# Performance work log

Measured on AMD Instinct MI355X. Metric: run time of the kernel, lower is better.

Reference implementation:

```python
import jax, jax.numpy as jnp
import numpy as np

N_NODES = 50000
N_EDGES = 800000
NODE_IN = 5
EDGE_IN = 1
HID = 64


def setup_inputs() -> dict:
    key = jax.random.key(0)
    ks = jax.random.split(key, 16)
    x = jax.random.normal(ks[0], (N_NODES, NODE_IN), dtype=jnp.float32)
    edge_index = jax.random.randint(ks[1], (2, N_EDGES), 0, N_NODES, dtype=jnp.int32)
    edge_attr = jax.random.normal(ks[2], (N_EDGES, EDGE_IN), dtype=jnp.float32)
    def lin(k, fan_in, fan_out):
        b = 1.0 / np.sqrt(fan_in)
        k1, k2 = jax.random.split(k)
        W = jax.random.uniform(k1, (fan_in, fan_out), minval=-b, maxval=b, dtype=jnp.float32)
        bi = jax.random.uniform(k2, (fan_out,), minval=-b, maxval=b, dtype=jnp.float32)
        return W, bi
    W_ne, b_ne = lin(ks[3], NODE_IN, HID)
    W_ee, b_ee = lin(ks[4], EDGE_IN, HID)
    W_gcn, b_gcn = lin(ks[5], HID, HID)   # PyG GCNConv: lin (no bias) + separate bias
    W1, b1 = lin(ks[6], 3 * HID, HID)
    W2, b2 = lin(ks[7], HID, 1)
    return {"x": x, "edge_index": edge_index, "edge_attr": edge_attr,
            "W_ne": W_ne, "b_ne": b_ne, "W_ee": W_ee, "b_ee": b_ee,
            "W_gcn": W_gcn, "b_gcn": b_gcn, "W1": W1, "b1": b1, "W2": W2, "b2": b2}


def gcn_conv(h, edge_index, W, b):
    # PyG GCNConv: add self-loops, symmetric norm D^-1/2 (A+I) D^-1/2, linear, scatter-add.
    N = h.shape[0]
    src, dst = edge_index[0], edge_index[1]
    loops = jnp.arange(N, dtype=src.dtype)
    row = jnp.concatenate([src, loops])  # message sources
    col = jnp.concatenate([dst, loops])  # message targets
    deg = jax.ops.segment_sum(jnp.ones(col.shape[0], h.dtype), col, num_segments=N)
    dinv = jnp.where(deg > 0, jax.lax.rsqrt(deg), 0.0)
    norm = dinv[row] * dinv[col]          # [E+N]
    ht = h @ W                            # [N, HID]
    msg = ht[row] * norm[:, None]         # gather + scale
    return jax.ops.segment_sum(msg, col, num_segments=N) + b


def reference(x, edge_index, edge_attr, W_ne, b_ne, W_ee, b_ee, W_gcn, b_gcn, W1, b1, W2, b2):
    h = jax.nn.relu(x @ W_ne + b_ne)                    # node encoder
    ef = jax.nn.relu(edge_attr @ W_ee + b_ee)           # edge encoder
    h = gcn_conv(h, edge_index, W_gcn, b_gcn)           # GCN layer
    src, dst = edge_index[0], edge_index[1]
    edge_input = jnp.concatenate([h[src], h[dst], ef], axis=1)  # [E, 3*HID]
    out = jax.nn.relu(edge_input @ W1 + b1) @ W2 + b2   # edge MLP -> [E, 1]
    return out.reshape(-1)
```

## Files before the change

kernel.cpp:

```cpp
#include <hip/hip_runtime.h>

#define NN 50000
#define NE 800000
#define H  64
#define NBKT 196
#define BCAP 8192
#define BIN_CHUNK 2048

typedef __attribute__((ext_vector_type(8))) short bf16x8;
typedef __attribute__((ext_vector_type(4))) float f32x4;

__device__ __forceinline__ unsigned short f2bf(float f) {
  unsigned int u = __builtin_bit_cast(unsigned int, f);
  u += 0x7FFFu + ((u >> 16) & 1u);
  return (unsigned short)(u >> 16);
}
__device__ __forceinline__ float bf2f(unsigned short u) {
  unsigned int v = ((unsigned int)u) << 16;
  return __builtin_bit_cast(float, v);
}

__global__ __launch_bounds__(256) void k_prep(
    const float* __restrict__ W1, const float* __restrict__ b1,
    const float* __restrict__ W_ee, const float* __restrict__ b_ee,
    float* __restrict__ thrS, float* __restrict__ cT,
    unsigned short* __restrict__ w1f, int* __restrict__ gcur) {
  const int t = threadIdx.x;
  if (blockIdx.x == 2) {
    if (t < NBKT) gcur[t] = 0;
    return;
  }
  if (blockIdx.x == 1) {
    const int ln = t & 63, q = t >> 6;
    const int l15_ = ln & 15, l4_ = ln >> 4;
#pragma unroll
    for (int f = 0; f < 4; ++f) {
      const int idx = q * 4 + f;
      const int g = idx >> 3;
      const int ct = (idx >> 1) & 3;
      const int c = idx & 1;
#pragma unroll
      for (int j = 0; j < 8; ++j) {
        const int k = g * 64 + c * 32 + l4_ * 8 + j;
        const int hcol = ct * 16 + l15_;
        w1f[(idx * 64 + ln) * 8 + j] = f2bf(W1[k * H + hcol]);
      }
    }
    return;
  }
  __shared__ float swee[64], sbee[64], sth[64];
  __shared__ int skx[64];
  if (t < 64) {
    const float w = W_ee[t], b = b_ee[t];
    swee[t] = w; sbee[t] = b;
    sth[t] = (w != 0.f) ? (-b / w) : __builtin_inff();
    skx[t] = t;
  }
  __syncthreads();
  for (int sz = 2; sz <= 64; sz <<= 1)
    for (int st = sz >> 1; st > 0; st >>= 1) {
      if (t < 64) {
        const int p = t ^ st;
        if (p > t) {
          const bool up = ((t & sz) == 0);
          const float a = sth[t], bb = sth[p];
          if (up ? (a > bb) : (a < bb)) {
            const int ka = skx[t];
            sth[t] = bb; sth[p] = a;
            skx[t] = skx[p]; skx[p] = ka;
          }
        }
      }
      __syncthreads();
    }
  if (t < 64) {
    const int h = t;
    float c1 = 0.f, c0 = b1[h];
    for (int k = 0; k < 64; ++k) {
      const float w = swee[k], b = sbee[k];
      if (w < 0.f || (w == 0.f && b > 0.f)) {
        const float wv1 = W1[(128 + k) * H + h];
        c1 = fmaf(w, wv1, c1);
        c0 = fmaf(b, wv1, c0);
      }
    }
    float2* cT2 = (float2*)cT;
    cT2[h] = make_float2(c1, c0);
    for (int iv = 1; iv <= 64; ++iv) {
      const int ks = skx[iv - 1];
      const float w = swee[ks];
      const float s = (w > 0.f) ? 1.f : -1.f;
      const float wv1 = W1[(128 + ks) * H + h];
      c1 = fmaf(s * w, wv1, c1);
      c0 = fmaf(s * sbee[ks], wv1, c0);
      cT2[iv * 66 + h] = make_float2(c1, c0);
    }
    thrS[h] = sth[h];
  }
}

__global__ __launch_bounds__(256) void k_bin(const int* __restrict__ ei,
                                             unsigned int* __restrict__ gbin,
                                             int* __restrict__ gcur) {
  __shared__ int hist[NBKT], base[NBKT];
  const int t = threadIdx.x;
  if (t < NBKT) hist[t] = 0;
  __syncthreads();

  const int e0 = blockIdx.x * BIN_CHUNK;
  int srcv[8], dstv[8], loff[8];
#pragma unroll
  for (int j = 0; j < 8; ++j) {
    const int e = e0 + j * 256 + t;
    if (e < NE) {
      srcv[j] = ei[e];
      dstv[j] = ei[NE + e];
      loff[j] = atomicAdd(&hist[dstv[j] >> 8], 1);
    } else dstv[j] = -1;
  }
  __syncthreads();
  if (t < NBKT) base[t] = atomicAdd(&gcur[t], hist[t]);
  __syncthreads();
#pragma unroll
  for (int j = 0; j < 8; ++j) {
    if (dstv[j] >= 0) {
      const int b = dstv[j] >> 8;
      const int pos = base[b] + loff[j];
      if (pos < BCAP)
        gbin[(size_t)b * BCAP + pos] =
            ((unsigned int)srcv[j] << 8) | (unsigned int)(dstv[j] & 255);
    }
  }
}

__global__ __launch_bounds__(256) void k_pass2(const unsigned int* __restrict__ gbin,
                                               const int* __restrict__ gcur,
                                               unsigned short* __restrict__ gcsr,
                                               int2* __restrict__ rowrange,
                                               float* __restrict__ dinv) {
  __shared__ int hist[256], cur[256], sc[256];
  __shared__ unsigned short lcsr[BCAP];
  const int b = blockIdx.x, t = threadIdx.x;
  const int sz = min(gcur[b], BCAP);
  hist[t] = 0;
  __syncthreads();

  const unsigned int* bb = gbin + (size_t)b * BCAP;
  for (int i = t; i < sz; i += 256) atomicAdd(&hist[bb[i] & 255], 1);
  __syncthreads();

  int v = hist[t];
  const int cnt = v;
  sc[t] = v;
  __syncthreads();
#pragma unroll
  for (int off = 1; off < 256; off <<= 1) {
    const int o = (t >= off) ? sc[t - off] : 0;
    __syncthreads();
    v += o;
    sc[t] = v;
    __syncthreads();
  }
  const int ex = v - cnt;
  cur[t] = ex;
  const int d = b * 256 + t;
  if (d < NN) {
    const int beg = b * BCAP + ex;
    rowrange[d] = make_int2(beg, beg + cnt);
    dinv[d] = rsqrtf((float)(cnt + 1));
  }
  __syncthreads();

  for (int i = t; i < sz; i += 256) {
    const unsigned int en = bb[i];
    const int off = atomicAdd(&cur[en & 255], 1);
    lcsr[off] = (unsigned short)(en >> 8);
  }
  __syncthreads();
  for (int i = t; i < sz; i += 256) gcsr[(size_t)b * BCAP + i] = lcsr[i];
}

__global__ __launch_bounds__(256) void k_node(
    const float* __restrict__ x, const float* __restrict__ W_ne,
    const float* __restrict__ b_ne, const float* __restrict__ W_gcn,
    const float* __restrict__ dinv, unsigned short* __restrict__ htb) {
  __shared__ float sh[4][H];
  const int lane = threadIdx.x & 63;
  const int wv   = threadIdx.x >> 6;
  const int n    = blockIdx.x * 4 + wv;

  float acc = b_ne[lane];
#pragma unroll
  for (int k = 0; k < 5; ++k) acc = fmaf(x[n * 5 + k], W_ne[k * H + lane], acc);
  acc = fmaxf(acc, 0.0f);
  sh[wv][lane] = acc;
  __syncthreads();

  float hv = 0.0f;
#pragma unroll 8
  for (int k = 0; k < H; ++k) hv = fmaf(sh[wv][k], W_gcn[k * H + lane], hv);

  htb[(size_t)n * H + lane] = f2bf(hv * dinv[n]);
}

__global__ __launch_bounds__(256) void k_gather(
    const int2* __restrict__ rowrange, const unsigned short* __restrict__ gcsr,
    const unsigned short* __restrict__ htb, const float* __restrict__ dinv,
    const float* __restrict__ b_gcn, unsigned short* __restrict__ hgb) {
  const int lane = threadIdx.x & 63;
  const int wv   = threadIdx.x >> 6;
  const int n    = blockIdx.x * 4 + wv;
  const int2 rr = rowrange[n];

  float sum = bf2f(htb[(size_t)n * H + lane]);
  int i = rr.x;
#pragma unroll 1
  for (; i + 4 <= rr.y; i += 4) {
    const int s0 = gcsr[i], s1 = gcsr[i + 1];
    const int s2 = gcsr[i + 2], s3 = gcsr[i + 3];
    const float v0 = bf2f(htb[(size_t)s0 * H + lane]);
    const float v1 = bf2f(htb[(size_t)s1 * H + lane]);
    const float v2 = bf2f(htb[(size_t)s2 * H + lane]);
    const float v3 = bf2f(htb[(size_t)s3 * H + lane]);
    sum += (v0 + v1) + (v2 + v3);
  }
#pragma unroll 1
  for (; i < rr.y; ++i) sum += bf2f(htb[(size_t)gcsr[i] * H + lane]);

  hgb[(size_t)n * H + lane] = f2bf(fmaf(dinv[n], sum, b_gcn[lane]));
}

__global__ __launch_bounds__(256) void k_uv(const unsigned short* __restrict__ hgb,
                                            const unsigned short* __restrict__ w1f,
                                            unsigned short* __restrict__ u,
                                            unsigned short* __restrict__ v) {
  const int lane = threadIdx.x & 63;
  const int wv   = threadIdx.x >> 6;
  const int tile = blockIdx.x * 4 + wv;
  if (tile >= NN / 16) return;
  const int n0 = tile * 16;
  const int l15 = lane & 15, l4 = lane >> 4;

  const unsigned short* ap = hgb + (size_t)(n0 + l15) * H + l4 * 8;
  const bf16x8 a0 = *(const bf16x8*)(ap);
  const bf16x8 a1 = *(const bf16x8*)(ap + 32);

  bf16x8 bU[4][2], bV[4][2];
#pragma unroll
  for (int ct = 0; ct < 4; ++ct)
#pragma unroll
    for (int c = 0; c < 2; ++c) {
      bU[ct][c] = *(const bf16x8*)(w1f + ((0 + ct * 2 + c) * 64 + lane) * 8);
      bV[ct][c] = *(const bf16x8*)(w1f + ((8 + ct * 2 + c) * 64 + lane) * 8);
    }

  f32x4 au[4], av[4];
#pragma unroll
  for (int ct = 0; ct < 4; ++ct) {
    au[ct] = (f32x4)(0.f);
    av[ct] = (f32x4)(0.f);
    au[ct] = __builtin_amdgcn_mfma_f32_16x16x32_bf16(a0, bU[ct][0], au[ct], 0, 0, 0);
    au[ct] = __builtin_amdgcn_mfma_f32_16x16x32_bf16(a1, bU[ct][1], au[ct], 0, 0, 0);
    av[ct] = __builtin_amdgcn_mfma_f32_16x16x32_bf16(a0, bV[ct][0], av[ct], 0, 0, 0);
    av[ct] = __builtin_amdgcn_mfma_f32_16x16x32_bf16(a1, bV[ct][1], av[ct], 0, 0, 0);
  }

#pragma unroll
  for (int ct = 0; ct < 4; ++ct)
#pragma unroll
    for (int r = 0; r < 4; ++r) {
      const size_t idx = (size_t)(n0 + l4 * 4 + r) * H + ct * 16 + l15;
      u[idx] = f2bf(au[ct][r]);
      v[idx] = f2bf(av[ct][r]);
    }
}

#define ET 5
__global__ __launch_bounds__(256) void k_edge(
    const int* __restrict__ ei, const float* __restrict__ eattr,
    const unsigned short* __restrict__ u, const unsigned short* __restrict__ v,
    const float* __restrict__ thrS, const float* __restrict__ cT,
    const float* __restrict__ W2, const float* __restrict__ b2,
    float* __restrict__ out) {
  __shared__ float sThr[64];
  __shared__ float sCT[65 * 132];

  const int t = threadIdx.x;
  if (t < 64) sThr[t] = thrS[t];
  for (int i = t; i < 65 * 66; i += 256)
    ((float2*)sCT)[i] = ((const float2*)cT)[i];
  __syncthreads();

  const int lane = t & 63;
  const int wv   = t >> 6;
  const int l15  = lane & 15, l4 = lane >> 4;
  const float b2v = b2[0];

  float w2v[16];
#pragma unroll
  for (int j = 0; j < 16; ++j) w2v[j] = W2[l4 * 16 + j];

  const int tile0 = (blockIdx.x * 4 + wv) * ET;
#pragma unroll 1
  for (int tt = 0; tt < ET; ++tt) {
    const int eBase = (tile0 + tt) * 16;
    const int src = ei[eBase + l15];
    const int dst = ei[NE + eBase + l15];
    const float ea = eattr[eBase + l15];

    unsigned int ud[8], vd[8];
    {
      const unsigned short* up = u + (size_t)src * H + l4 * 16;
      const unsigned short* vp = v + (size_t)dst * H + l4 * 16;
      *(uint4*)(ud)     = *(const uint4*)(up);
      *(uint4*)(ud + 4) = *(const uint4*)(up + 8);
      *(uint4*)(vd)     = *(const uint4*)(vp);
      *(uint4*)(vd + 4) = *(const uint4*)(vp + 8);
    }

    int iv = 0;
#pragma unroll
    for (int st = 64; st >= 1; st >>= 1) {
      const int nc = iv + st;
      if (nc <= 64 && sThr[nc - 1] <= ea) iv = nc;
    }

    const float* cp = sCT + iv * 132 + l4 * 32;
    float p = 0.0f;
#pragma unroll
    for (int r = 0; r < 8; ++r) {
      const float4 cc = *(const float4*)(cp + r * 4);
      const float ulo = __builtin_bit_cast(float, ud[r] << 16);
      const float uhi = __builtin_bit_cast(float, ud[r] & 0xFFFF0000u);
      const float vlo = __builtin_bit_cast(float, vd[r] << 16);
      const float vhi = __builtin_bit_cast(float, vd[r] & 0xFFFF0000u);
      const float z0 = ulo + vlo + fmaf(ea, cc.x, cc.y);
      const float z1 = uhi + vhi + fmaf(ea, cc.z, cc.w);
      p = fmaf(fmaxf(z0, 0.f), w2v[2 * r], p);
      p = fmaf(fmaxf(z1, 0.f), w2v[2 * r + 1], p);
    }

    p += __shfl_xor(p, 16);
    p += __shfl_xor(p, 32);
    if (lane < 16) out[eBase + lane] = p + b2v;
  }
}

extern "C" void kernel_launch(void* const* d_in, const int* in_sizes, int n_in,
                              void* d_out, int out_size, void* d_ws, size_t ws_size,
                              hipStream_t stream) {
  const float* x     = (const float*)d_in[0];
  const int*   ei    = (const int*)d_in[1];
  const float* eattr = (const float*)d_in[2];
  const float* W_ne  = (const float*)d_in[3];
  const float* b_ne  = (const float*)d_in[4];
  const float* W_ee  = (const float*)d_in[5];
  const float* b_ee  = (const float*)d_in[6];
  const float* W_gcn = (const float*)d_in[7];
  const float* b_gcn = (const float*)d_in[8];
  const float* W1    = (const float*)d_in[9];
  const float* b1    = (const float*)d_in[10];
  const float* W2    = (const float*)d_in[11];
  const float* b2    = (const float*)d_in[12];
  float* out = (float*)d_out;

  char* ws = (char*)d_ws;
  unsigned short* htb = (unsigned short*)(ws + 0);
  unsigned short* hgb = (unsigned short*)(ws + 6400000);
  unsigned int*   gbin = (unsigned int*)(ws + 12800000);
  unsigned short* vT  = (unsigned short*)(ws + 12800000);
  unsigned short* gcsr = (unsigned short*)(ws + 19222528);
  int2*  rowrange = (int2*)(ws + 22433792);
  float* dinv    = (float*)(ws + 22833792);
  int*   gcur    = (int*)(ws + 23033792);
  float* thrS    = (float*)(ws + 23034592);
  float* cT      = (float*)(ws + 23034848);
  unsigned short* w1f = (unsigned short*)(ws + 23069168);
  unsigned short* uT  = htb;

  k_prep<<<3, 256, 0, stream>>>(W1, b1, W_ee, b_ee, thrS, cT, w1f, gcur);
  k_bin<<<(NE + BIN_CHUNK - 1) / BIN_CHUNK, 256, 0, stream>>>(ei, gbin, gcur);
  k_pass2<<<NBKT, 256, 0, stream>>>(gbin, gcur, gcsr, rowrange, dinv);
  k_node<<<NN / 4, 256, 0, stream>>>(x, W_ne, b_ne, W_gcn, dinv, htb);
  k_gather<<<NN / 4, 256, 0, stream>>>(rowrange, gcsr, htb, dinv, b_gcn, hgb);
  k_uv<<<(NN / 16 + 3) / 4, 256, 0, stream>>>(hgb, w1f, uT, vT);
  k_edge<<<NE / (4 * ET * 16), 256, 0, stream>>>(ei, eattr, uT, vT, thrS, cT, W2, b2, out);
}
```

Baseline: 171.5 us.

## Fuse GCN gather with u/v MFMA projection and software-pipeline edge loads

Merges the neighbor-aggregation kernel and the u/v MFMA projection into one kernel. Each block of 16 nodes aggregates into a swizzled LDS tile, which feeds the MFMAs directly, so the hgb round trip through global memory and one launch go away. Each wave now handles 4 nodes sequentially, and the 4 waves split the output column tiles. The edge kernel now preloads all indices and double-buffers the u/v gathers to overlap loads with compute, at the cost of more registers and less gather parallelism per block.

```diff
diff --git a/kernel.cpp b/kernel.cpp
--- a/kernel.cpp
+++ b/kernel.cpp
@@ -203,76 +203,101 @@
   htb[(size_t)n * H + lane] = f2bf(hv * dinv[n]);
 }
 
-__global__ __launch_bounds__(256) void k_gather(
+__global__ __launch_bounds__(256) void k_gather_uv(
     const int2* __restrict__ rowrange, const unsigned short* __restrict__ gcsr,
     const unsigned short* __restrict__ htb, const float* __restrict__ dinv,
-    const float* __restrict__ b_gcn, unsigned short* __restrict__ hgb) {
+    const float* __restrict__ b_gcn, const unsigned short* __restrict__ w1f,
+    unsigned short* __restrict__ u, unsigned short* __restrict__ v) {
+  __shared__ unsigned short shg[16 * 64];
   const int lane = threadIdx.x & 63;
   const int wv   = threadIdx.x >> 6;
-  const int n    = blockIdx.x * 4 + wv;
-  const int2 rr = rowrange[n];
-
-  float sum = bf2f(htb[(size_t)n * H + lane]);
-  int i = rr.x;
+  const int n0   = blockIdx.x * 16;
+  const float bg = b_gcn[lane];
+
 #pragma unroll 1
-  for (; i + 4 <= rr.y; i += 4) {
-    const int s0 = gcsr[i], s1 = gcsr[i + 1];
-    const int s2 = gcsr[i + 2], s3 = gcsr[i + 3];
-    const float v0 = bf2f(htb[(size_t)s0 * H + lane]);
-    const float v1 = bf2f(htb[(size_t)s1 * H + lane]);
-    const float v2 = bf2f(htb[(size_t)s2 * H + lane]);
-    const float v3 = bf2f(htb[(size_t)s3 * H + lane]);
-    sum += (v0 + v1) + (v2 + v3);
-  }
+  for (int q = 0; q < 4; ++q) {
+    const int nl = wv * 4 + q;
+    const int n  = n0 + nl;
+    const int2 rr = rowrange[n];
+    float sum = bf2f(htb[(size_t)n * H + lane]);
+    int i = rr.x;
 #pragma unroll 1
-  for (; i < rr.y; ++i) sum += bf2f(htb[(size_t)gcsr[i] * H + lane]);
-
-  hgb[(size_t)n * H + lane] = f2bf(fmaf(dinv[n], sum, b_gcn[lane]));
-}
-
-__global__ __launch_bounds__(256) void k_uv(const unsigned short* __restrict__ hgb,
-                                            const unsigned short* __restrict__ w1f,
-                                            unsigned short* __restrict__ u,
-                                            unsigned short* __restrict__ v) {
-  const int lane = threadIdx.x & 63;
-  const int wv   = threadIdx.x >> 6;
-  const int tile = blockIdx.x * 4 + wv;
-  if (tile >= NN / 16) return;
-  const int n0 = tile * 16;
+    for (; i + 4 <= rr.y; i += 4) {
+      const int s0 = gcsr[i], s1 = gcsr[i + 1];
+      const int s2 = gcsr[i + 2], s3 = gcsr[i + 3];
+      const float v0 = bf2f(htb[(size_t)s0 * H + lane]);
+      const float v1 = bf2f(htb[(size_t)s1 * H + lane]);
+      const float v2 = bf2f(htb[(size_t)s2 * H + lane]);
+      const float v3 = bf2f(htb[(size_t)s3 * H + lane]);
+      sum += (v0 + v1) + (v2 + v3);
+    }
+#pragma unroll 1
+    for (; i < rr.y; ++i) sum += bf2f(htb[(size_t)gcsr[i] * H + lane]);
+
+    const float hgv = fmaf(dinv[n], sum, bg);
+    shg[((nl * 128 + lane * 2) ^ ((nl & 7) << 4)) >> 1] = f2bf(hgv);
+  }
+  __syncthreads();
+
   const int l15 = lane & 15, l4 = lane >> 4;
-
-  const unsigned short* ap = hgb + (size_t)(n0 + l15) * H + l4 * 8;
-  const bf16x8 a0 = *(const bf16x8*)(ap);
-  const bf16x8 a1 = *(const bf16x8*)(ap + 32);
-
-  bf16x8 bU[4][2], bV[4][2];
-#pragma unroll
-  for (int ct = 0; ct < 4; ++ct)
-#pragma unroll
-    for (int c = 0; c < 2; ++c) {
-      bU[ct][c] = *(const bf16x8*)(w1f + ((0 + ct * 2 + c) * 64 + lane) * 8);
-      bV[ct][c] = *(const bf16x8*)(w1f + ((8 + ct * 2 + c) * 64 + lane) * 8);
-    }
-
-  f32x4 au[4], av[4];
-#pragma unroll
-  for (int ct = 0; ct < 4; ++ct) {
-    au[ct] = (f32x4)(0.f);
-    av[ct] = (f32x4)(0.f);
-    au[ct] = __builtin_amdgcn_mfma_f32_16x16x32_bf16(a0, bU[ct][0], au[ct], 0, 0, 0);
-    au[ct] = __builtin_amdgcn_mfma_f32_16x16x32_bf16(a1, bU[ct][1], au[ct], 0, 0, 0);
-    av[ct] = __builtin_amdgcn_mfma_f32_16x16x32_bf16(a0, bV[ct][0], av[ct], 0, 0, 0);
-    av[ct] = __builtin_amdgcn_mfma_f32_16x16x32_bf16(a1, bV[ct][1], av[ct], 0, 0, 0);
-  }
-
-#pragma unroll
-  for (int ct = 0; ct < 4; ++ct)
-#pragma unroll
-    for (int r = 0; r < 4; ++r) {
-      const size_t idx = (size_t)(n0 + l4 * 4 + r) * H + ct * 16 + l15;
-      u[idx] = f2bf(au[ct][r]);
-      v[idx] = f2bf(av[ct][r]);
-    }
+  const bf16x8 a0 = *(const bf16x8*)(shg + (((l15 * 128 + l4 * 16) ^ ((l15 & 7) << 4)) >> 1));
+  const bf16x8 a1 = *(const bf16x8*)(shg + (((l15 * 128 + 64 + l4 * 16) ^ ((l15 & 7) << 4)) >> 1));
+
+  const int ct = wv;
+  const bf16x8 bu0 = *(const bf16x8*)(w1f + ((ct * 2 + 0) * 64 + lane) * 8);
+  const bf16x8 bu1 = *(const bf16x8*)(w1f + ((ct * 2 + 1) * 64 + lane) * 8);
+  const bf16x8 bv0 = *(const bf16x8*)(w1f + ((8 + ct * 2 + 0) * 64 + lane) * 8);
+  const bf16x8 bv1 = *(const bf16x8*)(w1f + ((8 + ct * 2 + 1) * 64 + lane) * 8);
+
+  f32x4 au = (f32x4)(0.f), av = (f32x4)(0.f);
+  au = __builtin_amdgcn_mfma_f32_16x16x32_bf16(a0, bu0, au, 0, 0, 0);
+  au = __builtin_amdgcn_mfma_f32_16x16x32_bf16(a1, bu1, au, 0, 0, 0);
+  av = __builtin_amdgcn_mfma_f32_16x16x32_bf16(a0, bv0, av, 0, 0, 0);
+  av = __builtin_amdgcn_mfma_f32_16x16x32_bf16(a1, bv1, av, 0, 0, 0);
+
+#pragma unroll
+  for (int r = 0; r < 4; ++r) {
+    const size_t idx = (size_t)(n0 + l4 * 4 + r) * H + ct * 16 + l15;
+    u[idx] = f2bf(au[r]);
+    v[idx] = f2bf(av[r]);
+  }
+}
+
+__device__ __forceinline__ int find_iv(const float* __restrict__ sThr, float ea) {
+  int iv = 0;
+#pragma unroll
+  for (int st = 64; st >= 1; st >>= 1) {
+    const int nc = iv + st;
+    if (nc <= 64 && sThr[nc - 1] <= ea) iv = nc;
+  }
+  return iv;
+}
+
+__device__ __forceinline__ void edge_compute(
+    float ea, uint4 U0, uint4 U1, uint4 V0, uint4 V1,
+    const float* __restrict__ sThr, const float* __restrict__ sCT,
+    const float* __restrict__ w2v, int l4, int lane, float b2v,
+    float* __restrict__ out, int obase) {
+  const int iv = find_iv(sThr, ea);
+  const float* cp = sCT + iv * 132 + l4 * 32;
+  const unsigned int ud[8] = {U0.x, U0.y, U0.z, U0.w, U1.x, U1.y, U1.z, U1.w};
+  const unsigned int vd[8] = {V0.x, V0.y, V0.z, V0.w, V1.x, V1.y, V1.z, V1.w};
+  float p = 0.f;
+#pragma unroll
+  for (int r = 0; r < 8; ++r) {
+    const float4 cc = *(const float4*)(cp + r * 4);
+    const float ulo = __builtin_bit_cast(float, ud[r] << 16);
+    const float uhi = __builtin_bit_cast(float, ud[r] & 0xFFFF0000u);
+    const float vlo = __builtin_bit_cast(float, vd[r] << 16);
+    const float vhi = __builtin_bit_cast(float, vd[r] & 0xFFFF0000u);
+    const float z0 = ulo + vlo + fmaf(ea, cc.x, cc.y);
+    const float z1 = uhi + vhi + fmaf(ea, cc.z, cc.w);
+    p = fmaf(fmaxf(z0, 0.f), w2v[2 * r], p);
+    p = fmaf(fmaxf(z1, 0.f), w2v[2 * r + 1], p);
+  }
+  p += __shfl_xor(p, 16);
+  p += __shfl_xor(p, 32);
+  if (lane < 16) out[obase + lane] = p + b2v;
 }
 
 #define ET 5
@@ -301,49 +326,34 @@
   for (int j = 0; j < 16; ++j) w2v[j] = W2[l4 * 16 + j];
 
   const int tile0 = (blockIdx.x * 4 + wv) * ET;
-#pragma unroll 1
+  int srcA[ET], dstA[ET];
+  float eaA[ET];
+#pragma unroll
   for (int tt = 0; tt < ET; ++tt) {
-    const int eBase = (tile0 + tt) * 16;
-    const int src = ei[eBase + l15];
-    const int dst = ei[NE + eBase + l15];
-    const float ea = eattr[eBase + l15];
-
-    unsigned int ud[8], vd[8];
-    {
-      const unsigned short* up = u + (size_t)src * H + l4 * 16;
-      const unsigned short* vp = v + (size_t)dst * H + l4 * 16;
-      *(uint4*)(ud)     = *(const uint4*)(up);
-      *(uint4*)(ud + 4) = *(const uint4*)(up + 8);
-      *(uint4*)(vd)     = *(const uint4*)(vp);
-      *(uint4*)(vd + 4) = *(const uint4*)(vp + 8);
-    }
-
-    int iv = 0;
-#pragma unroll
-    for (int st = 64; st >= 1; st >>= 1) {
-      const int nc = iv + st;
-      if (nc <= 64 && sThr[nc - 1] <= ea) iv = nc;
-    }
-
-    const float* cp = sCT + iv * 132 + l4 * 32;
-    float p = 0.0f;
-#pragma unroll
-    for (int r = 0; r < 8; ++r) {
-      const float4 cc = *(const float4*)(cp + r * 4);
-      const float ulo = __builtin_bit_cast(float, ud[r] << 16);
-      const float uhi = __builtin_bit_cast(float, ud[r] & 0xFFFF0000u);
-      const float vlo = __builtin_bit_cast(float, vd[r] << 16);
-      const float vhi = __builtin_bit_cast(float, vd[r] & 0xFFFF0000u);
-      const float z0 = ulo + vlo + fmaf(ea, cc.x, cc.y);
-      const float z1 = uhi + vhi + fmaf(ea, cc.z, cc.w);
-      p = fmaf(fmaxf(z0, 0.f), w2v[2 * r], p);
-      p = fmaf(fmaxf(z1, 0.f), w2v[2 * r + 1], p);
-    }
-
-    p += __shfl_xor(p, 16);
-    p += __shfl_xor(p, 32);
-    if (lane < 16) out[eBase + lane] = p + b2v;
-  }
+    srcA[tt] = ei[(tile0 + tt) * 16 + l15];
+    dstA[tt] = ei[NE + (tile0 + tt) * 16 + l15];
+    eaA[tt]  = eattr[(tile0 + tt) * 16 + l15];
+  }
+
+  uint4 Au0, Au1, Av0, Av1, Bu0, Bu1, Bv0, Bv1;
+
+#define LOADUV(U0, U1, V0, V1, tt) {                              \
+    const unsigned short* up = u + (size_t)srcA[tt] * H + l4 * 16; \
+    const unsigned short* vp = v + (size_t)dstA[tt] * H + l4 * 16; \
+    U0 = *(const uint4*)(up); U1 = *(const uint4*)(up + 8);        \
+    V0 = *(const uint4*)(vp); V1 = *(const uint4*)(vp + 8); }
+
+  LOADUV(Au0, Au1, Av0, Av1, 0);
+  LOADUV(Bu0, Bu1, Bv0, Bv1, 1);
+  edge_compute(eaA[0], Au0, Au1, Av0, Av1, sThr, sCT, w2v, l4, lane, b2v, out, (tile0 + 0) * 16);
+  LOADUV(Au0, Au1, Av0, Av1, 2);
+  edge_compute(eaA[1], Bu0, Bu1, Bv0, Bv1, sThr, sCT, w2v, l4, lane, b2v, out, (tile0 + 1) * 16);
+  LOADUV(Bu0, Bu1, Bv0, Bv1, 3);
+  edge_compute(eaA[2], Au0, Au1, Av0, Av1, sThr, sCT, w2v, l4, lane, b2v, out, (tile0 + 2) * 16);
+  LOADUV(Au0, Au1, Av0, Av1, 4);
+  edge_compute(eaA[3], Bu0, Bu1, Bv0, Bv1, sThr, sCT, w2v, l4, lane, b2v, out, (tile0 + 3) * 16);
+  edge_compute(eaA[4], Au0, Au1, Av0, Av1, sThr, sCT, w2v, l4, lane, b2v, out, (tile0 + 4) * 16);
+#undef LOADUV
 }
 
 extern "C" void kernel_launch(void* const* d_in, const int* in_sizes, int n_in,
@@ -366,7 +376,7 @@
 
   char* ws = (char*)d_ws;
   unsigned short* htb = (unsigned short*)(ws + 0);
-  unsigned short* hgb = (unsigned short*)(ws + 6400000);
+  unsigned short* uT  = (unsigned short*)(ws + 6400000);
   unsigned int*   gbin = (unsigned int*)(ws + 12800000);
   unsigned short* vT  = (unsigned short*)(ws + 12800000);
   unsigned short* gcsr = (unsigned short*)(ws + 19222528);
@@ -376,13 +386,11 @@
   float* thrS    = (float*)(ws + 23034592);
   float* cT      = (float*)(ws + 23034848);
   unsigned short* w1f = (unsigned short*)(ws + 23069168);
-  unsigned short* uT  = htb;
 
   k_prep<<<3, 256, 0, stream>>>(W1, b1, W_ee, b_ee, thrS, cT, w1f, gcur);
   k_bin<<<(NE + BIN_CHUNK - 1) / BIN_CHUNK, 256, 0, stream>>>(ei, gbin, gcur);
   k_pass2<<<NBKT, 256, 0, stream>>>(gbin, gcur, gcsr, rowrange, dinv);
   k_node<<<NN / 4, 256, 0, stream>>>(x, W_ne, b_ne, W_gcn, dinv, htb);
-  k_gather<<<NN / 4, 256, 0, stream>>>(rowrange, gcsr, htb, dinv, b_gcn, hgb);
-  k_uv<<<(NN / 16 + 3) / 4, 256, 0, stream>>>(hgb, w1f, uT, vT);
+  k_gather_uv<<<NN / 16, 256, 0, stream>>>(rowrange, gcsr, htb, dinv, b_gcn, w1f, uT, vT);
   k_edge<<<NE / (4 * ET * 16), 256, 0, stream>>>(ei, eattr, uT, vT, thrS, cT, W2, b2, out);
 }
```

Measured after the change: 159.4 us. -7.1%, faster.
